# Kernel optimization log

Hardware: AMD Instinct MI355X
Metric: run time of the kernel (lower is better)

Reference implementation:

```python
import jax, jax.numpy as jnp
import numpy as np

D_MODEL = 1024
N_HEADS = 16
D_K = D_MODEL // N_HEADS


def setup_inputs() -> dict:
    key = jax.random.key(0)
    ks = jax.random.split(key, 11)
    B, S, D = 2, 2048, D_MODEL
    scale = 1.0 / np.sqrt(D)
    inp = {
        "q": jax.random.normal(ks[0], (B, S, D), jnp.float32),
        "k": jax.random.normal(ks[1], (B, S, D), jnp.float32),
        "v": jax.random.normal(ks[2], (B, S, D), jnp.float32),
        "wq": jax.random.normal(ks[3], (D, D), jnp.float32) * scale,
        "bq": jax.random.normal(ks[4], (D,), jnp.float32) * 0.01,
        "wk": jax.random.normal(ks[5], (D, D), jnp.float32) * scale,
        "bk": jax.random.normal(ks[6], (D,), jnp.float32) * 0.01,
        "wv": jax.random.normal(ks[7], (D, D), jnp.float32) * scale,
        "bv": jax.random.normal(ks[8], (D,), jnp.float32) * 0.01,
        "wo": jax.random.normal(ks[9], (D, D), jnp.float32) * scale,
        "bo": jax.random.normal(ks[10], (D,), jnp.float32) * 0.01,
    }
    return inp


def _split_heads(x, B):
    # [B, S, D] -> [B, H, S, d_k]
    return x.reshape(B, -1, N_HEADS, D_K).transpose(0, 2, 1, 3)


def reference(q, k, v, wq, bq, wk, bk, wv, bv, wo, bo):
    B, S, D = q.shape
    # Linear projections (torch Linear: x @ W^T + b)
    qh = _split_heads(q @ wq.T + bq, B)  # [B,H,S,dk]
    kh = _split_heads(k @ wk.T + bk, B)
    vh = _split_heads(v @ wv.T + bv, B)
    scores = jnp.einsum("bhqd,bhkd->bhqk", qh, kh) / jnp.sqrt(jnp.float32(D_K))
    attn = jax.nn.softmax(scores, axis=-1)  # [B,H,S,S]
    out = jnp.einsum("bhqk,bhkd->bhqd", attn, vh)  # [B,H,S,dk]
    out = out.transpose(0, 2, 1, 3).reshape(B, S, D)
    out = out @ wo.T + bo
    return (out, attn)
```

## Files before the change

kernel.cpp:

```cpp
#include <hip/hip_runtime.h>

#define D_MODEL 1024
#define N_HEADS 16
#define D_K     64
#define BB      2
#define SS      2048
#define M_TOT   (BB * SS)

typedef __attribute__((ext_vector_type(8))) short short8;
typedef __attribute__((ext_vector_type(4))) float f32x4;

__device__ __forceinline__ unsigned short bf_rne(float x) {
    unsigned u = __builtin_bit_cast(unsigned, x);
    u += 0x7fff + ((u >> 16) & 1);
    return (unsigned short)(u >> 16);
}
__device__ __forceinline__ void split2(float x, unsigned short& h, unsigned short& l) {
    unsigned short hh = bf_rne(x);
    float hf = __builtin_bit_cast(float, ((unsigned)hh) << 16);
    l = bf_rne(x - hf);
    h = hh;
}

__device__ __forceinline__ int swz(int r, int k) {
    return r * 64 + ((((k >> 3) ^ (r & 7)) << 3) | (k & 7));
}

__global__ __launch_bounds__(256) void split_f32(
    const float* __restrict__ in, unsigned short* __restrict__ h,
    unsigned short* __restrict__ l, int n4)
{
    int i = blockIdx.x * 256 + threadIdx.x;
    if (i >= n4) return;
    float4 v = ((const float4*)in)[i];
    unsigned short hh[4], ll[4];
    split2(v.x, hh[0], ll[0]); split2(v.y, hh[1], ll[1]);
    split2(v.z, hh[2], ll[2]); split2(v.w, hh[3], ll[3]);
    *(ushort4*)&h[i * 4] = make_ushort4(hh[0], hh[1], hh[2], hh[3]);
    *(ushort4*)&l[i * 4] = make_ushort4(ll[0], ll[1], ll[2], ll[3]);
}

template <int STORE, bool BIAS>
__global__ __launch_bounds__(256, 2) void gemm3(
    const float* __restrict__ A, int lda,
    const unsigned short* __restrict__ Bh, const unsigned short* __restrict__ Bl,
    int ldb,
    const float* __restrict__ bias,
    float* __restrict__ Cf, unsigned short* __restrict__ Ch,
    unsigned short* __restrict__ Cl,
    int ldc, int K)
{
    const int m0 = blockIdx.y * 128;
    const int n0 = blockIdx.x * 128;
    const int t  = threadIdx.x;
    const int lane = t & 63;
    const int wy = t >> 7;
    const int wx = (t >> 6) & 1;

    __shared__ __align__(16) unsigned short Ahs[128 * 64];
    __shared__ __align__(16) unsigned short Als[128 * 64];
    __shared__ __align__(16) unsigned short Bhs[128 * 64];
    __shared__ __align__(16) unsigned short Bls[128 * 64];

    const int sr = t >> 3;
    const int sc = (t & 7) * 8;

    f32x4 acc[4][4];
#pragma unroll
    for (int i = 0; i < 4; ++i)
#pragma unroll
        for (int j = 0; j < 4; ++j) acc[i][j] = (f32x4){0.f, 0.f, 0.f, 0.f};

    for (int k0 = 0; k0 < K; k0 += 64) {
        float4 a0[4], a1[4];
#pragma unroll
        for (int p = 0; p < 4; ++p) {
            const float* s = &A[(long)(m0 + sr + 32 * p) * lda + k0 + sc];
            a0[p] = *(const float4*)s;
            a1[p] = *(const float4*)(s + 4);
        }
        short8 gbh[4], gbl[4];
#pragma unroll
        for (int p = 0; p < 4; ++p) {
            const long bo = (long)(n0 + sr + 32 * p) * ldb + k0 + sc;
            gbh[p] = *(const short8*)&Bh[bo];
            gbl[p] = *(const short8*)&Bl[bo];
        }
        __syncthreads();
#pragma unroll
        for (int p = 0; p < 4; ++p) {
            union { short8 v; unsigned short u[8]; } ph, pl;
            float f[8] = {a0[p].x, a0[p].y, a0[p].z, a0[p].w,
                          a1[p].x, a1[p].y, a1[p].z, a1[p].w};
#pragma unroll
            for (int e = 0; e < 8; ++e) split2(f[e], ph.u[e], pl.u[e]);
            const int idx = swz(sr + 32 * p, sc);
            *(short8*)&Ahs[idx] = ph.v;
            *(short8*)&Als[idx] = pl.v;
            *(short8*)&Bhs[idx] = gbh[p];
            *(short8*)&Bls[idx] = gbl[p];
        }
        __syncthreads();

#pragma unroll
        for (int ks = 0; ks < 2; ++ks) {
            const int fr = lane & 15;
            const int fk = ks * 32 + (lane >> 4) * 8;
            short8 ah[4], al[4], bh8[4], bl8[4];
#pragma unroll
            for (int i = 0; i < 4; ++i) {
                const int idx = swz(wy * 64 + i * 16 + fr, fk);
                ah[i] = *(const short8*)&Ahs[idx];
                al[i] = *(const short8*)&Als[idx];
            }
#pragma unroll
            for (int j = 0; j < 4; ++j) {
                const int idx = swz(wx * 64 + j * 16 + fr, fk);
                bh8[j] = *(const short8*)&Bhs[idx];
                bl8[j] = *(const short8*)&Bls[idx];
            }
#pragma unroll
            for (int i = 0; i < 4; ++i)
#pragma unroll
                for (int j = 0; j < 4; ++j) {
                    acc[i][j] = __builtin_amdgcn_mfma_f32_16x16x32_bf16(ah[i], bh8[j], acc[i][j], 0, 0, 0);
                    acc[i][j] = __builtin_amdgcn_mfma_f32_16x16x32_bf16(al[i], bh8[j], acc[i][j], 0, 0, 0);
                    acc[i][j] = __builtin_amdgcn_mfma_f32_16x16x32_bf16(ah[i], bl8[j], acc[i][j], 0, 0, 0);
                }
        }
    }

    const int fr = lane & 15;
    const int fq = lane >> 4;
#pragma unroll
    for (int j = 0; j < 4; ++j) {
        const int n = n0 + wx * 64 + j * 16 + fr;
        const float bj = BIAS ? bias[n] : 0.0f;
#pragma unroll
        for (int i = 0; i < 4; ++i)
#pragma unroll
            for (int r = 0; r < 4; ++r) {
                const int m = m0 + wy * 64 + i * 16 + fq * 4 + r;
                const float val = acc[i][j][r] + bj;
                if (STORE == 0) {
                    Cf[(long)m * ldc + n] = val;
                } else if (STORE == 2) {
                    const int b = m >> 11, s = m & 2047, h = n >> 6, d = n & 63;
                    unsigned short hh, ll; split2(val, hh, ll);
                    const long idx = (((long)(b * N_HEADS + h)) * SS + s) * 64 + d;
                    Ch[idx] = hh; Cl[idx] = ll;
                } else {
                    const int b = m >> 11, s = m & 2047, h = n >> 6, d = n & 63;
                    unsigned short hh, ll; split2(val, hh, ll);
                    const long idx = (((long)(b * N_HEADS + h)) * 64 + d) * SS + s;
                    Ch[idx] = hh; Cl[idx] = ll;
                }
            }
    }
}

__global__ __launch_bounds__(256, 2) void attn_fused(
    const unsigned short* __restrict__ qh_hi, const unsigned short* __restrict__ qh_lo,
    const unsigned short* __restrict__ kh_hi, const unsigned short* __restrict__ kh_lo,
    const unsigned short* __restrict__ vt_hi, const unsigned short* __restrict__ vt_lo,
    float* __restrict__ attn, float* __restrict__ oh)
{
    const int z  = blockIdx.x;
    const int m0 = blockIdx.y * 128;
    const int b  = z >> 4;
    const int h  = z & 15;
    const int t  = threadIdx.x;
    const int lane = t & 63;
    const int wy = t >> 7;
    const int wx = (t >> 6) & 1;
    const int fr = lane & 15;
    const int fg = lane >> 4;

    __shared__ __align__(16) unsigned short Qh[128 * 64];
    __shared__ __align__(16) unsigned short Ql[128 * 64];
    __shared__ __align__(16) unsigned short Wh[128 * 64];
    __shared__ __align__(16) unsigned short Wl[128 * 64];
    __shared__ float red_m[2][128];
    __shared__ float red_l[2][128];
    __shared__ float sm_m[128];
    __shared__ float sm_rl[128];

    const int sr = t >> 3;
    const int sc = (t & 7) * 8;

    float* attnZ = attn + (long)z * SS * SS;

#pragma unroll
    for (int p = 0; p < 4; ++p) {
        const long g = ((long)z * SS + m0 + sr + 32 * p) * 64 + sc;
        *(short8*)&Qh[swz(sr + 32 * p, sc)] = *(const short8*)&qh_hi[g];
        *(short8*)&Ql[swz(sr + 32 * p, sc)] = *(const short8*)&qh_lo[g];
    }

    float m_reg[16], l_reg[16];
#pragma unroll
    for (int e = 0; e < 16; ++e) { m_reg[e] = -3.0e38f; l_reg[e] = 0.f; }

    for (int nt = 0; nt < 16; ++nt) {
        const int j0 = nt * 128;
        short8 kh8[4], kl8[4];
#pragma unroll
        for (int p = 0; p < 4; ++p) {
            const long g = ((long)z * SS + j0 + sr + 32 * p) * 64 + sc;
            kh8[p] = *(const short8*)&kh_hi[g];
            kl8[p] = *(const short8*)&kh_lo[g];
        }
        __syncthreads();
#pragma unroll
        for (int p = 0; p < 4; ++p) {
            const int idx = swz(sr + 32 * p, sc);
            *(short8*)&Wh[idx] = kh8[p];
            *(short8*)&Wl[idx] = kl8[p];
        }
        __syncthreads();

        f32x4 acc[4][4];
#pragma unroll
        for (int i = 0; i < 4; ++i)
#pragma unroll
            for (int j = 0; j < 4; ++j) acc[i][j] = (f32x4){0.f, 0.f, 0.f, 0.f};

#pragma unroll
        for (int ks = 0; ks < 2; ++ks) {
            const int fk = ks * 32 + fg * 8;
            short8 ah[4], al[4], bh8[4], bl8[4];
#pragma unroll
            for (int i = 0; i < 4; ++i) {
                const int idx = swz(wy * 64 + i * 16 + fr, fk);
                ah[i] = *(const short8*)&Qh[idx];
                al[i] = *(const short8*)&Ql[idx];
            }
#pragma unroll
            for (int j = 0; j < 4; ++j) {
                const int idx = swz(wx * 64 + j * 16 + fr, fk);
                bh8[j] = *(const short8*)&Wh[idx];
                bl8[j] = *(const short8*)&Wl[idx];
            }
#pragma unroll
            for (int i = 0; i < 4; ++i)
#pragma unroll
                for (int j = 0; j < 4; ++j) {
                    acc[i][j] = __builtin_amdgcn_mfma_f32_16x16x32_bf16(ah[i], bh8[j], acc[i][j], 0, 0, 0);
                    acc[i][j] = __builtin_amdgcn_mfma_f32_16x16x32_bf16(al[i], bh8[j], acc[i][j], 0, 0, 0);
                    acc[i][j] = __builtin_amdgcn_mfma_f32_16x16x32_bf16(ah[i], bl8[j], acc[i][j], 0, 0, 0);
                }
        }

#pragma unroll
        for (int i = 0; i < 4; ++i)
#pragma unroll
            for (int j = 0; j < 4; ++j) acc[i][j] *= 0.125f;

#pragma unroll
        for (int i = 0; i < 4; ++i)
#pragma unroll
            for (int r = 0; r < 4; ++r) {
                const int e = i * 4 + r;
                const float tmax = fmaxf(fmaxf(acc[i][0][r], acc[i][1][r]),
                                         fmaxf(acc[i][2][r], acc[i][3][r]));
                const float mO = m_reg[e];
                const float mN = fmaxf(mO, tmax);
                const float s = __expf(acc[i][0][r] - mN) + __expf(acc[i][1][r] - mN)
                              + __expf(acc[i][2][r] - mN) + __expf(acc[i][3][r] - mN);
                l_reg[e] = l_reg[e] * __expf(mO - mN) + s;
                m_reg[e] = mN;
            }

#pragma unroll
        for (int i = 0; i < 4; ++i)
#pragma unroll
            for (int r = 0; r < 4; ++r) {
                const long row = (long)(m0 + wy * 64 + i * 16 + fg * 4 + r) * SS;
#pragma unroll
                for (int j = 0; j < 4; ++j)
                    attnZ[row + j0 + wx * 64 + j * 16 + fr] = acc[i][j][r];
            }
    }

#pragma unroll
    for (int e = 0; e < 16; ++e) {
        float mm = m_reg[e], ll = l_reg[e];
#pragma unroll
        for (int off = 1; off < 16; off <<= 1) {
            const float mo = __shfl_xor(mm, off);
            const float lo = __shfl_xor(ll, off);
            const float M = fmaxf(mm, mo);
            ll = ll * __expf(mm - M) + lo * __expf(mo - M);
            mm = M;
        }
        m_reg[e] = mm; l_reg[e] = ll;
    }
    if (fr == 0) {
#pragma unroll
        for (int e = 0; e < 16; ++e) {
            const int row = wy * 64 + (e >> 2) * 16 + fg * 4 + (e & 3);
            red_m[wx][row] = m_reg[e];
            red_l[wx][row] = l_reg[e];
        }
    }
    __syncthreads();
    if (t < 128) {
        const float ma = red_m[0][t], mb = red_m[1][t];
        const float M = fmaxf(ma, mb);
        const float L = red_l[0][t] * __expf(ma - M) + red_l[1][t] * __expf(mb - M);
        sm_m[t] = M;
        sm_rl[t] = 1.0f / L;
    }
    __syncthreads();

    f32x4 oacc[4][2];
#pragma unroll
    for (int i = 0; i < 4; ++i)
#pragma unroll
        for (int j = 0; j < 2; ++j) oacc[i][j] = (f32x4){0.f, 0.f, 0.f, 0.f};

    for (int k0 = 0; k0 < SS; k0 += 64) {
        float4 a0[4], a1[4];
#pragma unroll
        for (int p = 0; p < 4; ++p) {
            const float* src = &attnZ[(long)(m0 + sr + 32 * p) * SS + k0 + sc];
            a0[p] = *(const float4*)src;
            a1[p] = *(const float4*)(src + 4);
        }
        short8 vh8[2], vl8[2];
#pragma unroll
        for (int p = 0; p < 2; ++p) {
            const long g = ((long)z * 64 + sr + 32 * p) * SS + k0 + sc;
            vh8[p] = *(const short8*)&vt_hi[g];
            vl8[p] = *(const short8*)&vt_lo[g];
        }
        __syncthreads();
#pragma unroll
        for (int p = 0; p < 4; ++p) {
            const int rl_ = sr + 32 * p;
            const float mR = sm_m[rl_], rR = sm_rl[rl_];
            float f[8] = {a0[p].x, a0[p].y, a0[p].z, a0[p].w,
                          a1[p].x, a1[p].y, a1[p].z, a1[p].w};
            union { short8 v; unsigned short u[8]; } ph, pl;
            float pv[8];
#pragma unroll
            for (int e = 0; e < 8; ++e) {
                pv[e] = __expf(f[e] - mR) * rR;
                split2(pv[e], ph.u[e], pl.u[e]);
            }
            float* dst = &attnZ[(long)(m0 + rl_) * SS + k0 + sc];
            *(float4*)dst = make_float4(pv[0], pv[1], pv[2], pv[3]);
            *(float4*)(dst + 4) = make_float4(pv[4], pv[5], pv[6], pv[7]);
            const int idx = swz(rl_, sc);
            *(short8*)&Wh[idx] = ph.v;
            *(short8*)&Wl[idx] = pl.v;
        }
#pragma unroll
        for (int p = 0; p < 2; ++p) {
            const int idx = swz(sr + 32 * p, sc);
            *(short8*)&Qh[idx] = vh8[p];
            *(short8*)&Ql[idx] = vl8[p];
        }
        __syncthreads();

#pragma unroll
        for (int ks = 0; ks < 2; ++ks) {
            const int fk = ks * 32 + fg * 8;
            short8 pa_h[4], pa_l[4], vb_h[2], vb_l[2];
#pragma unroll
            for (int i = 0; i < 4; ++i) {
                const int idx = swz(wy * 64 + i * 16 + fr, fk);
                pa_h[i] = *(const short8*)&Wh[idx];
                pa_l[i] = *(const short8*)&Wl[idx];
            }
#pragma unroll
            for (int jn = 0; jn < 2; ++jn) {
                const int idx = swz(wx * 32 + jn * 16 + fr, fk);
                vb_h[jn] = *(const short8*)&Qh[idx];
                vb_l[jn] = *(const short8*)&Ql[idx];
            }
#pragma unroll
            for (int i = 0; i < 4; ++i)
#pragma unroll
                for (int jn = 0; jn < 2; ++jn) {
                    oacc[i][jn] = __builtin_amdgcn_mfma_f32_16x16x32_bf16(pa_h[i], vb_h[jn], oacc[i][jn], 0, 0, 0);
                    oacc[i][jn] = __builtin_amdgcn_mfma_f32_16x16x32_bf16(pa_l[i], vb_h[jn], oacc[i][jn], 0, 0, 0);
                    oacc[i][jn] = __builtin_amdgcn_mfma_f32_16x16x32_bf16(pa_h[i], vb_l[jn], oacc[i][jn], 0, 0, 0);
                }
        }
    }

#pragma unroll
    for (int jn = 0; jn < 2; ++jn) {
        const int d = wx * 32 + jn * 16 + fr;
#pragma unroll
        for (int i = 0; i < 4; ++i)
#pragma unroll
            for (int r = 0; r < 4; ++r) {
                const int m = m0 + wy * 64 + i * 16 + fg * 4 + r;
                oh[((long)(b * SS + m)) * D_MODEL + h * 64 + d] = oacc[i][jn][r];
            }
    }
}

extern "C" void kernel_launch(void* const* d_in, const int* in_sizes, int n_in,
                              void* d_out, int out_size, void* d_ws, size_t ws_size,
                              hipStream_t stream)
{
    const float* q  = (const float*)d_in[0];
    const float* k  = (const float*)d_in[1];
    const float* v  = (const float*)d_in[2];
    const float* wq = (const float*)d_in[3];
    const float* bq = (const float*)d_in[4];
    const float* wk = (const float*)d_in[5];
    const float* bk = (const float*)d_in[6];
    const float* wv = (const float*)d_in[7];
    const float* bv = (const float*)d_in[8];
    const float* wo = (const float*)d_in[9];
    const float* bo = (const float*)d_in[10];

    float* out  = (float*)d_out;
    float* attn = out + (long)BB * SS * D_MODEL;

    char* ws = (char*)d_ws;
    unsigned short* qh_hi = (unsigned short*)ws;
    unsigned short* qh_lo = (unsigned short*)(ws + (8L  << 20));
    unsigned short* kh_hi = (unsigned short*)(ws + (16L << 20));
    unsigned short* kh_lo = (unsigned short*)(ws + (24L << 20));
    unsigned short* vt_hi = (unsigned short*)(ws + (32L << 20));
    unsigned short* vt_lo = (unsigned short*)(ws + (40L << 20));
    float*          oh    = (float*)(ws + (48L << 20));
    unsigned short* wq_hi = (unsigned short*)(ws + (48L << 20));
    unsigned short* wq_lo = (unsigned short*)(ws + (50L << 20));
    unsigned short* wk_hi = (unsigned short*)(ws + (52L << 20));
    unsigned short* wk_lo = (unsigned short*)(ws + (54L << 20));
    unsigned short* wv_hi = (unsigned short*)(ws + (56L << 20));
    unsigned short* wv_lo = (unsigned short*)(ws + (58L << 20));
    unsigned short* wo_hi = (unsigned short*)(ws);
    unsigned short* wo_lo = (unsigned short*)(ws + (2L << 20));

    const dim3 blk(256);
    const int NW4 = (D_MODEL * D_MODEL) / 4;

    hipLaunchKernelGGL(split_f32, dim3(1024), blk, 0, stream, wq, wq_hi, wq_lo, NW4);
    hipLaunchKernelGGL(split_f32, dim3(1024), blk, 0, stream, wk, wk_hi, wk_lo, NW4);
    hipLaunchKernelGGL(split_f32, dim3(1024), blk, 0, stream, wv, wv_hi, wv_lo, NW4);

    const dim3 gproj(D_MODEL / 128, M_TOT / 128, 1);
    hipLaunchKernelGGL((gemm3<2, true>), gproj, blk, 0, stream,
                       q, D_MODEL, wq_hi, wq_lo, D_MODEL, bq,
                       (float*)nullptr, qh_hi, qh_lo, 0, D_MODEL);
    hipLaunchKernelGGL((gemm3<2, true>), gproj, blk, 0, stream,
                       k, D_MODEL, wk_hi, wk_lo, D_MODEL, bk,
                       (float*)nullptr, kh_hi, kh_lo, 0, D_MODEL);
    hipLaunchKernelGGL((gemm3<3, true>), gproj, blk, 0, stream,
                       v, D_MODEL, wv_hi, wv_lo, D_MODEL, bv,
                       (float*)nullptr, vt_hi, vt_lo, 0, D_MODEL);

    hipLaunchKernelGGL(attn_fused, dim3(BB * N_HEADS, SS / 128), blk, 0, stream,
                       qh_hi, qh_lo, kh_hi, kh_lo, vt_hi, vt_lo, attn, oh);

    hipLaunchKernelGGL(split_f32, dim3(1024), blk, 0, stream, wo, wo_hi, wo_lo, NW4);

    hipLaunchKernelGGL((gemm3<0, true>), gproj, blk, 0, stream,
                       oh, D_MODEL, wo_hi, wo_lo, D_MODEL, bo,
                       out, (unsigned short*)nullptr, (unsigned short*)nullptr,
                       D_MODEL, D_MODEL);
}
```

Before: 1.148 ms.

## Recompute QK^T in second pass instead of round-tripping raw scores through attn

Pass one now only computes the softmax row max and sum, with no score writes to global memory. Pass two recomputes QK^T per 64-key tile, writes the normalized probabilities once with nontemporal stores, and feeds the PV MFMAs from a packed hi/lo LDS buffer. Q fragments stay in registers and V fragments are loaded directly from global memory. This removes a full write and re-read of the large attention matrix at the cost of doing the split-bf16 QK MFMAs twice and using more registers.

```diff
diff --git a/kernel.cpp b/kernel.cpp
--- a/kernel.cpp
+++ b/kernel.cpp
@@ -176,110 +176,86 @@
     const int fr = lane & 15;
     const int fg = lane >> 4;
 
-    __shared__ __align__(16) unsigned short Qh[128 * 64];
-    __shared__ __align__(16) unsigned short Ql[128 * 64];
-    __shared__ __align__(16) unsigned short Wh[128 * 64];
-    __shared__ __align__(16) unsigned short Wl[128 * 64];
+    __shared__ __align__(16) unsigned short Kh[64 * 64];
+    __shared__ __align__(16) unsigned short Kl[64 * 64];
+    __shared__ __align__(16) unsigned int   Pb[128 * 64];
     __shared__ float red_m[2][128];
     __shared__ float red_l[2][128];
     __shared__ float sm_m[128];
     __shared__ float sm_rl[128];
 
-    const int sr = t >> 3;
-    const int sc = (t & 7) * 8;
-
     float* attnZ = attn + (long)z * SS * SS;
 
-#pragma unroll
-    for (int p = 0; p < 4; ++p) {
-        const long g = ((long)z * SS + m0 + sr + 32 * p) * 64 + sc;
-        *(short8*)&Qh[swz(sr + 32 * p, sc)] = *(const short8*)&qh_hi[g];
-        *(short8*)&Ql[swz(sr + 32 * p, sc)] = *(const short8*)&qh_lo[g];
-    }
+    short8 qa_h[2][4], qa_l[2][4];
+#pragma unroll
+    for (int ks = 0; ks < 2; ++ks)
+#pragma unroll
+        for (int i = 0; i < 4; ++i) {
+            const long g = ((long)z * SS + m0 + wy * 64 + i * 16 + fr) * 64 + ks * 32 + fg * 8;
+            qa_h[ks][i] = *(const short8*)&qh_hi[g];
+            qa_l[ks][i] = *(const short8*)&qh_lo[g];
+        }
+
+    const int krow = t >> 2;
+    const int kc   = (t & 3) * 16;
 
     float m_reg[16], l_reg[16];
 #pragma unroll
     for (int e = 0; e < 16; ++e) { m_reg[e] = -3.0e38f; l_reg[e] = 0.f; }
 
-    for (int nt = 0; nt < 16; ++nt) {
-        const int j0 = nt * 128;
-        short8 kh8[4], kl8[4];
-#pragma unroll
-        for (int p = 0; p < 4; ++p) {
-            const long g = ((long)z * SS + j0 + sr + 32 * p) * 64 + sc;
-            kh8[p] = *(const short8*)&kh_hi[g];
-            kl8[p] = *(const short8*)&kh_lo[g];
-        }
-        __syncthreads();
-#pragma unroll
-        for (int p = 0; p < 4; ++p) {
-            const int idx = swz(sr + 32 * p, sc);
-            *(short8*)&Wh[idx] = kh8[p];
-            *(short8*)&Wl[idx] = kl8[p];
-        }
-        __syncthreads();
-
-        f32x4 acc[4][4];
-#pragma unroll
-        for (int i = 0; i < 4; ++i)
-#pragma unroll
-            for (int j = 0; j < 4; ++j) acc[i][j] = (f32x4){0.f, 0.f, 0.f, 0.f};
+    for (int nt = 0; nt < 32; ++nt) {
+        const int j0 = nt * 64;
+        const long gk = ((long)z * SS + j0 + krow) * 64 + kc;
+        const short8 g0h = *(const short8*)&kh_hi[gk];
+        const short8 g1h = *(const short8*)&kh_hi[gk + 8];
+        const short8 g0l = *(const short8*)&kh_lo[gk];
+        const short8 g1l = *(const short8*)&kh_lo[gk + 8];
+        *(short8*)&Kh[swz(krow, kc)]     = g0h;
+        *(short8*)&Kh[swz(krow, kc + 8)] = g1h;
+        *(short8*)&Kl[swz(krow, kc)]     = g0l;
+        *(short8*)&Kl[swz(krow, kc + 8)] = g1l;
+        __syncthreads();
+
+        f32x4 acc[4][2];
+#pragma unroll
+        for (int i = 0; i < 4; ++i) { acc[i][0] = (f32x4){0,0,0,0}; acc[i][1] = (f32x4){0,0,0,0}; }
 
 #pragma unroll
         for (int ks = 0; ks < 2; ++ks) {
             const int fk = ks * 32 + fg * 8;
-            short8 ah[4], al[4], bh8[4], bl8[4];
-#pragma unroll
-            for (int i = 0; i < 4; ++i) {
-                const int idx = swz(wy * 64 + i * 16 + fr, fk);
-                ah[i] = *(const short8*)&Qh[idx];
-                al[i] = *(const short8*)&Ql[idx];
-            }
-#pragma unroll
-            for (int j = 0; j < 4; ++j) {
-                const int idx = swz(wx * 64 + j * 16 + fr, fk);
-                bh8[j] = *(const short8*)&Wh[idx];
-                bl8[j] = *(const short8*)&Wl[idx];
+            short8 bh8[2], bl8[2];
+#pragma unroll
+            for (int jf = 0; jf < 2; ++jf) {
+                const int idx = swz(wx * 32 + jf * 16 + fr, fk);
+                bh8[jf] = *(const short8*)&Kh[idx];
+                bl8[jf] = *(const short8*)&Kl[idx];
             }
 #pragma unroll
             for (int i = 0; i < 4; ++i)
 #pragma unroll
-                for (int j = 0; j < 4; ++j) {
-                    acc[i][j] = __builtin_amdgcn_mfma_f32_16x16x32_bf16(ah[i], bh8[j], acc[i][j], 0, 0, 0);
-                    acc[i][j] = __builtin_amdgcn_mfma_f32_16x16x32_bf16(al[i], bh8[j], acc[i][j], 0, 0, 0);
-                    acc[i][j] = __builtin_amdgcn_mfma_f32_16x16x32_bf16(ah[i], bl8[j], acc[i][j], 0, 0, 0);
-                }
-        }
-
-#pragma unroll
-        for (int i = 0; i < 4; ++i)
-#pragma unroll
-            for (int j = 0; j < 4; ++j) acc[i][j] *= 0.125f;
+                for (int jf = 0; jf < 2; ++jf) {
+                    acc[i][jf] = __builtin_amdgcn_mfma_f32_16x16x32_bf16(qa_h[ks][i], bh8[jf], acc[i][jf], 0, 0, 0);
+                    acc[i][jf] = __builtin_amdgcn_mfma_f32_16x16x32_bf16(qa_l[ks][i], bh8[jf], acc[i][jf], 0, 0, 0);
+                    acc[i][jf] = __builtin_amdgcn_mfma_f32_16x16x32_bf16(qa_h[ks][i], bl8[jf], acc[i][jf], 0, 0, 0);
+                }
+        }
+
+#pragma unroll
+        for (int i = 0; i < 4; ++i) { acc[i][0] *= 0.125f; acc[i][1] *= 0.125f; }
 
 #pragma unroll
         for (int i = 0; i < 4; ++i)
 #pragma unroll
             for (int r = 0; r < 4; ++r) {
                 const int e = i * 4 + r;
-                const float tmax = fmaxf(fmaxf(acc[i][0][r], acc[i][1][r]),
-                                         fmaxf(acc[i][2][r], acc[i][3][r]));
+                const float tmax = fmaxf(acc[i][0][r], acc[i][1][r]);
                 const float mO = m_reg[e];
                 const float mN = fmaxf(mO, tmax);
-                const float s = __expf(acc[i][0][r] - mN) + __expf(acc[i][1][r] - mN)
-                              + __expf(acc[i][2][r] - mN) + __expf(acc[i][3][r] - mN);
+                const float s = __expf(acc[i][0][r] - mN) + __expf(acc[i][1][r] - mN);
                 l_reg[e] = l_reg[e] * __expf(mO - mN) + s;
                 m_reg[e] = mN;
             }
-
-#pragma unroll
-        for (int i = 0; i < 4; ++i)
-#pragma unroll
-            for (int r = 0; r < 4; ++r) {
-                const long row = (long)(m0 + wy * 64 + i * 16 + fg * 4 + r) * SS;
-#pragma unroll
-                for (int j = 0; j < 4; ++j)
-                    attnZ[row + j0 + wx * 64 + j * 16 + fr] = acc[i][j][r];
-            }
+        __syncthreads();
     }
 
 #pragma unroll
@@ -315,90 +291,117 @@
 
     f32x4 oacc[4][2];
 #pragma unroll
-    for (int i = 0; i < 4; ++i)
-#pragma unroll
-        for (int j = 0; j < 2; ++j) oacc[i][j] = (f32x4){0.f, 0.f, 0.f, 0.f};
-
-    for (int k0 = 0; k0 < SS; k0 += 64) {
-        float4 a0[4], a1[4];
-#pragma unroll
-        for (int p = 0; p < 4; ++p) {
-            const float* src = &attnZ[(long)(m0 + sr + 32 * p) * SS + k0 + sc];
-            a0[p] = *(const float4*)src;
-            a1[p] = *(const float4*)(src + 4);
-        }
-        short8 vh8[2], vl8[2];
-#pragma unroll
-        for (int p = 0; p < 2; ++p) {
-            const long g = ((long)z * 64 + sr + 32 * p) * SS + k0 + sc;
-            vh8[p] = *(const short8*)&vt_hi[g];
-            vl8[p] = *(const short8*)&vt_lo[g];
-        }
-        __syncthreads();
-#pragma unroll
-        for (int p = 0; p < 4; ++p) {
-            const int rl_ = sr + 32 * p;
-            const float mR = sm_m[rl_], rR = sm_rl[rl_];
-            float f[8] = {a0[p].x, a0[p].y, a0[p].z, a0[p].w,
-                          a1[p].x, a1[p].y, a1[p].z, a1[p].w};
-            union { short8 v; unsigned short u[8]; } ph, pl;
-            float pv[8];
-#pragma unroll
-            for (int e = 0; e < 8; ++e) {
-                pv[e] = __expf(f[e] - mR) * rR;
-                split2(pv[e], ph.u[e], pl.u[e]);
-            }
-            float* dst = &attnZ[(long)(m0 + rl_) * SS + k0 + sc];
-            *(float4*)dst = make_float4(pv[0], pv[1], pv[2], pv[3]);
-            *(float4*)(dst + 4) = make_float4(pv[4], pv[5], pv[6], pv[7]);
-            const int idx = swz(rl_, sc);
-            *(short8*)&Wh[idx] = ph.v;
-            *(short8*)&Wl[idx] = pl.v;
-        }
-#pragma unroll
-        for (int p = 0; p < 2; ++p) {
-            const int idx = swz(sr + 32 * p, sc);
-            *(short8*)&Qh[idx] = vh8[p];
-            *(short8*)&Ql[idx] = vl8[p];
-        }
-        __syncthreads();
-
+    for (int i = 0; i < 4; ++i) { oacc[i][0] = (f32x4){0,0,0,0}; oacc[i][1] = (f32x4){0,0,0,0}; }
+
+    for (int nt = 0; nt < 32; ++nt) {
+        const int j0 = nt * 64;
+
+        const long gk = ((long)z * SS + j0 + krow) * 64 + kc;
+        const short8 g0h = *(const short8*)&kh_hi[gk];
+        const short8 g1h = *(const short8*)&kh_hi[gk + 8];
+        const short8 g0l = *(const short8*)&kh_lo[gk];
+        const short8 g1l = *(const short8*)&kh_lo[gk + 8];
+        short8 vb_h[2][2], vb_l[2][2];
+#pragma unroll
+        for (int nb = 0; nb < 2; ++nb)
+#pragma unroll
+            for (int ks = 0; ks < 2; ++ks) {
+                const long gv = ((long)z * 64 + wx * 32 + nb * 16 + fr) * SS + j0 + ks * 32 + fg * 8;
+                vb_h[nb][ks] = *(const short8*)&vt_hi[gv];
+                vb_l[nb][ks] = *(const short8*)&vt_lo[gv];
+            }
+
+        *(short8*)&Kh[swz(krow, kc)]     = g0h;
+        *(short8*)&Kh[swz(krow, kc + 8)] = g1h;
+        *(short8*)&Kl[swz(krow, kc)]     = g0l;
+        *(short8*)&Kl[swz(krow, kc + 8)] = g1l;
+        __syncthreads();
+
+        f32x4 acc[4][2];
+#pragma unroll
+        for (int i = 0; i < 4; ++i) { acc[i][0] = (f32x4){0,0,0,0}; acc[i][1] = (f32x4){0,0,0,0}; }
 #pragma unroll
         for (int ks = 0; ks < 2; ++ks) {
             const int fk = ks * 32 + fg * 8;
-            short8 pa_h[4], pa_l[4], vb_h[2], vb_l[2];
+            short8 bh8[2], bl8[2];
+#pragma unroll
+            for (int jf = 0; jf < 2; ++jf) {
+                const int idx = swz(wx * 32 + jf * 16 + fr, fk);
+                bh8[jf] = *(const short8*)&Kh[idx];
+                bl8[jf] = *(const short8*)&Kl[idx];
+            }
+#pragma unroll
+            for (int i = 0; i < 4; ++i)
+#pragma unroll
+                for (int jf = 0; jf < 2; ++jf) {
+                    acc[i][jf] = __builtin_amdgcn_mfma_f32_16x16x32_bf16(qa_h[ks][i], bh8[jf], acc[i][jf], 0, 0, 0);
+                    acc[i][jf] = __builtin_amdgcn_mfma_f32_16x16x32_bf16(qa_l[ks][i], bh8[jf], acc[i][jf], 0, 0, 0);
+                    acc[i][jf] = __builtin_amdgcn_mfma_f32_16x16x32_bf16(qa_h[ks][i], bl8[jf], acc[i][jf], 0, 0, 0);
+                }
+        }
+
+#pragma unroll
+        for (int i = 0; i < 4; ++i)
+#pragma unroll
+            for (int r = 0; r < 4; ++r) {
+                const int m_loc = wy * 64 + i * 16 + fg * 4 + r;
+                const float mR = sm_m[m_loc], rR = sm_rl[m_loc];
+                const long row = (long)(m0 + m_loc) * SS;
+#pragma unroll
+                for (int jf = 0; jf < 2; ++jf) {
+                    const int j_loc = wx * 32 + jf * 16 + fr;
+                    const float p = __expf(acc[i][jf][r] * 0.125f - mR) * rR;
+                    __builtin_nontemporal_store(p, &attnZ[row + j0 + j_loc]);
+                    unsigned short hh, ll; split2(p, hh, ll);
+                    const unsigned u = (unsigned)hh | ((unsigned)ll << 16);
+                    const int chunk = (j_loc >> 2) ^ (m_loc & 7);
+                    Pb[m_loc * 64 + (chunk << 2) + (j_loc & 3)] = u;
+                }
+            }
+        __syncthreads();
+
+#pragma unroll
+        for (int ks = 0; ks < 2; ++ks) {
+            short8 ph8[4], pl8[4];
 #pragma unroll
             for (int i = 0; i < 4; ++i) {
-                const int idx = swz(wy * 64 + i * 16 + fr, fk);
-                pa_h[i] = *(const short8*)&Wh[idx];
-                pa_l[i] = *(const short8*)&Wl[idx];
-            }
-#pragma unroll
-            for (int jn = 0; jn < 2; ++jn) {
-                const int idx = swz(wx * 32 + jn * 16 + fr, fk);
-                vb_h[jn] = *(const short8*)&Qh[idx];
-                vb_l[jn] = *(const short8*)&Ql[idx];
+                const int ml = wy * 64 + i * 16 + fr;
+                const int s8 = ml & 7;
+                const int base = ml * 64;
+                const int c0 = ks * 8 + fg * 2;
+                const uint4 clo = *(const uint4*)&Pb[base + ((c0 ^ s8) << 2)];
+                const uint4 chi = *(const uint4*)&Pb[base + (((c0 + 1) ^ s8) << 2)];
+                union { short8 v; unsigned u[4]; } hh, ll;
+                hh.u[0] = (clo.x & 0xffffu) | (clo.y << 16);
+                hh.u[1] = (clo.z & 0xffffu) | (clo.w << 16);
+                hh.u[2] = (chi.x & 0xffffu) | (chi.y << 16);
+                hh.u[3] = (chi.z & 0xffffu) | (chi.w << 16);
+                ll.u[0] = (clo.x >> 16) | (clo.y & 0xffff0000u);
+                ll.u[1] = (clo.z >> 16) | (clo.w & 0xffff0000u);
+                ll.u[2] = (chi.x >> 16) | (chi.y & 0xffff0000u);
+                ll.u[3] = (chi.z >> 16) | (chi.w & 0xffff0000u);
+                ph8[i] = hh.v; pl8[i] = ll.v;
             }
 #pragma unroll
             for (int i = 0; i < 4; ++i)
 #pragma unroll
-                for (int jn = 0; jn < 2; ++jn) {
-                    oacc[i][jn] = __builtin_amdgcn_mfma_f32_16x16x32_bf16(pa_h[i], vb_h[jn], oacc[i][jn], 0, 0, 0);
-                    oacc[i][jn] = __builtin_amdgcn_mfma_f32_16x16x32_bf16(pa_l[i], vb_h[jn], oacc[i][jn], 0, 0, 0);
-                    oacc[i][jn] = __builtin_amdgcn_mfma_f32_16x16x32_bf16(pa_h[i], vb_l[jn], oacc[i][jn], 0, 0, 0);
-                }
-        }
-    }
-
-#pragma unroll
-    for (int jn = 0; jn < 2; ++jn) {
-        const int d = wx * 32 + jn * 16 + fr;
+                for (int nb = 0; nb < 2; ++nb) {
+                    oacc[i][nb] = __builtin_amdgcn_mfma_f32_16x16x32_bf16(ph8[i], vb_h[nb][ks], oacc[i][nb], 0, 0, 0);
+                    oacc[i][nb] = __builtin_amdgcn_mfma_f32_16x16x32_bf16(pl8[i], vb_h[nb][ks], oacc[i][nb], 0, 0, 0);
+                    oacc[i][nb] = __builtin_amdgcn_mfma_f32_16x16x32_bf16(ph8[i], vb_l[nb][ks], oacc[i][nb], 0, 0, 0);
+                }
+        }
+    }
+
+#pragma unroll
+    for (int nb = 0; nb < 2; ++nb) {
+        const int d = wx * 32 + nb * 16 + fr;
 #pragma unroll
         for (int i = 0; i < 4; ++i)
 #pragma unroll
             for (int r = 0; r < 4; ++r) {
                 const int m = m0 + wy * 64 + i * 16 + fg * 4 + r;
-                oh[((long)(b * SS + m)) * D_MODEL + h * 64 + d] = oacc[i][jn][r];
+                oh[((long)(b * SS + m)) * D_MODEL + h * 64 + d] = oacc[i][nb][r];
             }
     }
 }
```

Result: slower. 1.281 ms (+11.6%).
